# Optimization experiments

Measured on AMD Instinct MI355X. Metric: run time of the kernel, lower is better.

## Reference

```python
import jax, jax.numpy as jnp
import numpy as np

NS = 150            # number of MC weight samples
D_IN, D_H, D_OUT = 1024, 512, 256


def setup_inputs() -> dict:
    key = jax.random.key(0)
    ks = jax.random.split(key, 9)
    x = jax.random.normal(ks[0], (32, D_IN), dtype=jnp.float32)
    # variational means (mu network params)
    mu_W1 = jax.random.normal(ks[1], (D_H, D_IN), dtype=jnp.float32) * 0.02
    mu_b1 = jnp.zeros((D_H,), dtype=jnp.float32)
    mu_W2 = jax.random.normal(ks[2], (D_OUT, D_H), dtype=jnp.float32) * 0.02
    mu_b2 = jnp.zeros((D_OUT,), dtype=jnp.float32)
    # variational log-stds (std network params v); std = exp(v)
    v_W1 = -3.0 + 0.1 * jax.random.normal(ks[3], (D_H, D_IN), dtype=jnp.float32)
    v_b1 = -3.0 + 0.1 * jax.random.normal(ks[4], (D_H,), dtype=jnp.float32)
    v_W2 = -3.0 + 0.1 * jax.random.normal(ks[5], (D_OUT, D_H), dtype=jnp.float32)
    v_b2 = -3.0 + 0.1 * jax.random.normal(ks[6], (D_OUT,), dtype=jnp.float32)
    return {
        "x": x,
        "mu_W1": mu_W1, "mu_b1": mu_b1, "mu_W2": mu_W2, "mu_b2": mu_b2,
        "v_W1": v_W1, "v_b1": v_b1, "v_W2": v_W2, "v_b2": v_b2,
    }


def reference(x, mu_W1, mu_b1, mu_W2, mu_b2, v_W1, v_b1, v_W2, v_b2):
    # Reparameterization: w = mu + eps * sqrt(exp(2v)) = mu + eps * exp(v)
    nk = jax.random.split(jax.random.key(42), 4)
    eW1 = jax.random.normal(nk[0], (NS,) + mu_W1.shape, dtype=mu_W1.dtype)
    eb1 = jax.random.normal(nk[1], (NS,) + mu_b1.shape, dtype=mu_b1.dtype)
    eW2 = jax.random.normal(nk[2], (NS,) + mu_W2.shape, dtype=mu_W2.dtype)
    eb2 = jax.random.normal(nk[3], (NS,) + mu_b2.shape, dtype=mu_b2.dtype)

    W1 = mu_W1 + eW1 * jnp.exp(v_W1)          # [ns, H, I]
    b1 = mu_b1 + eb1 * jnp.exp(v_b1)          # [ns, H]
    W2 = mu_W2 + eW2 * jnp.exp(v_W2)          # [ns, O, H]
    b2 = mu_b2 + eb2 * jnp.exp(v_b2)          # [ns, O]

    # MLP forward, batched over the ns sample axis
    h = jax.nn.relu(jnp.einsum('bi,nhi->nbh', x, W1) + b1[:, None, :])  # [ns, B, H]
    y = jnp.einsum('nbh,noh->nbo', h, W2) + b2[:, None, :]              # [ns, B, O]
    return y  # stacked MC outputs, [ns, B, O]
```

## Files before the change

### kernel.cpp

```cpp
#include <hip/hip_runtime.h>
#include <stdint.h>

#define NS 150
#define D_IN 1024
#define D_H 512
#define D_OUT 256

typedef __bf16 bf16x8 __attribute__((ext_vector_type(8)));
typedef float f32x4 __attribute__((ext_vector_type(4)));

#define OFF_XF    0u
#define OFF_MS1T  16384u
#define OFF_MS2T  1064960u
#define OFF_B1S   1327104u
#define OFF_B2S   1403904u
#define OFF_HB    1442304u

#define SQ2 1.41421354f

#define DSQ2 1.4142135623730951
#define DA  (-0.6931471805599453)
#define ZC3 ((float)(DSQ2 * -4.39150654e-06 * DA*DA*DA*DA*DA))
#define ZC4 ((float)(DSQ2 * 0.00021858087   * DA*DA*DA*DA))
#define ZC5 ((float)(DSQ2 * -0.00125372503  * DA*DA*DA))
#define ZC6 ((float)(DSQ2 * -0.00417768164  * DA*DA))
#define ZC7 ((float)(DSQ2 * 0.246640727     * DA))
#define ZC8 ((float)(DSQ2 * 1.50140941))
#define ZSHIFT 3.6067376022224085f
#define ZCUT  -7.213475204444817f

#define TT0 (SQ2 * -0.000200214257f)
#define TT1 (SQ2 * 0.000100950558f)
#define TT2 (SQ2 * 0.00134934322f)
#define TT3 (SQ2 * -0.00367342844f)
#define TT4 (SQ2 * 0.00573950773f)
#define TT5 (SQ2 * -0.0076224613f)
#define TT6 (SQ2 * 0.00943887047f)
#define TT7 (SQ2 * 1.00167406f)
#define TT8 (SQ2 * 2.83297682f)

#define ROTL32(x, r) __builtin_rotateleft32((x), (r))

__host__ __device__ __forceinline__ void threefry2x32(uint32_t k0, uint32_t k1,
                                                      uint32_t x0, uint32_t x1,
                                                      uint32_t& o0, uint32_t& o1) {
  uint32_t k2 = k0 ^ k1 ^ 0x1BD11BDAu;
  x0 += k0; x1 += k1;
#define TFR(r) { x0 += x1; x1 = ROTL32(x1, r); x1 ^= x0; }
  TFR(13) TFR(15) TFR(26) TFR(6)
  x0 += k1; x1 += k2 + 1u;
  TFR(17) TFR(29) TFR(16) TFR(24)
  x0 += k2; x1 += k0 + 2u;
  TFR(13) TFR(15) TFR(26) TFR(6)
  x0 += k0; x1 += k1 + 3u;
  TFR(17) TFR(29) TFR(16) TFR(24)
  x0 += k1; x1 += k2 + 4u;
  TFR(13) TFR(15) TFR(26) TFR(6)
  x0 += k2; x1 += k0 + 5u;
#undef TFR
  o0 = x0; o1 = x1;
}

__device__ __forceinline__ float tf_normal(uint32_t k0, uint32_t k1, uint32_t idx) {
  uint32_t o0, o1;
  threefry2x32(k0, k1, 0u, idx, o0, o1);
  uint32_t bits = o0 ^ o1;
  uint32_t fb = (bits >> 9) | 0x3F800000u;
  float m = __uint_as_float(fb);
  const float lo = -0.99999994f;
  float u = fmaxf(fmaf(m, 2.0f, -3.0f), lo);
  float t = fmaf(u, -u, 1.0f);
  float w = -0.69314718056f * __builtin_amdgcn_logf(t);
  float p;
  if (w < 5.0f) {
    float ww = w - 2.5f;
    p = SQ2 * 2.81022636e-08f;
    p = fmaf(p, ww, SQ2 * 3.43273939e-07f);
    p = fmaf(p, ww, SQ2 * -3.5233877e-06f);
    p = fmaf(p, ww, SQ2 * -4.39150654e-06f);
    p = fmaf(p, ww, SQ2 * 0.00021858087f);
    p = fmaf(p, ww, SQ2 * -0.00125372503f);
    p = fmaf(p, ww, SQ2 * -0.00417768164f);
    p = fmaf(p, ww, SQ2 * 0.246640727f);
    p = fmaf(p, ww, SQ2 * 1.50140941f);
  } else {
    float ww = __builtin_amdgcn_sqrtf(w) - 3.0f;
    p = TT0;
    p = fmaf(p, ww, TT1); p = fmaf(p, ww, TT2); p = fmaf(p, ww, TT3);
    p = fmaf(p, ww, TT4); p = fmaf(p, ww, TT5); p = fmaf(p, ww, TT6);
    p = fmaf(p, ww, TT7); p = fmaf(p, ww, TT8);
  }
  return p * u;
}

#define TF_ADD8 \
  "v_add_u32 %[a0], %[a0], %[b0]\n\t" "v_add_u32 %[a1], %[a1], %[b1]\n\t" \
  "v_add_u32 %[a2], %[a2], %[b2]\n\t" "v_add_u32 %[a3], %[a3], %[b3]\n\t" \
  "v_add_u32 %[a4], %[a4], %[b4]\n\t" "v_add_u32 %[a5], %[a5], %[b5]\n\t" \
  "v_add_u32 %[a6], %[a6], %[b6]\n\t" "v_add_u32 %[a7], %[a7], %[b7]\n\t"
#define TF_ROT8(sh) \
  "v_alignbit_b32 %[b0], %[b0], %[b0], " sh "\n\t" \
  "v_alignbit_b32 %[b1], %[b1], %[b1], " sh "\n\t" \
  "v_alignbit_b32 %[b2], %[b2], %[b2], " sh "\n\t" \
  "v_alignbit_b32 %[b3], %[b3], %[b3], " sh "\n\t" \
  "v_alignbit_b32 %[b4], %[b4], %[b4], " sh "\n\t" \
  "v_alignbit_b32 %[b5], %[b5], %[b5], " sh "\n\t" \
  "v_alignbit_b32 %[b6], %[b6], %[b6], " sh "\n\t" \
  "v_alignbit_b32 %[b7], %[b7], %[b7], " sh "\n\t"
#define TF_XOR8 \
  "v_xor_b32 %[b0], %[b0], %[a0]\n\t" "v_xor_b32 %[b1], %[b1], %[a1]\n\t" \
  "v_xor_b32 %[b2], %[b2], %[a2]\n\t" "v_xor_b32 %[b3], %[b3], %[a3]\n\t" \
  "v_xor_b32 %[b4], %[b4], %[a4]\n\t" "v_xor_b32 %[b5], %[b5], %[a5]\n\t" \
  "v_xor_b32 %[b6], %[b6], %[a6]\n\t" "v_xor_b32 %[b7], %[b7], %[a7]\n\t"
#define TF_ROUND(sh) TF_ADD8 TF_ROT8(sh) TF_XOR8
#define TF_R1(sh) \
  "v_add_u32 %[a0], %[k0], %[b0]\n\t" "v_add_u32 %[a1], %[k0], %[b1]\n\t" \
  "v_add_u32 %[a2], %[k0], %[b2]\n\t" "v_add_u32 %[a3], %[k0], %[b3]\n\t" \
  "v_add_u32 %[a4], %[k0], %[b4]\n\t" "v_add_u32 %[a5], %[k0], %[b5]\n\t" \
  "v_add_u32 %[a6], %[k0], %[b6]\n\t" "v_add_u32 %[a7], %[k0], %[b7]\n\t" \
  TF_ROT8(sh) TF_XOR8
#define TF_BADD8(KB) \
  "v_add_u32 %[b0], " KB ", %[b0]\n\t" "v_add_u32 %[b1], " KB ", %[b1]\n\t" \
  "v_add_u32 %[b2], " KB ", %[b2]\n\t" "v_add_u32 %[b3], " KB ", %[b3]\n\t" \
  "v_add_u32 %[b4], " KB ", %[b4]\n\t" "v_add_u32 %[b5], " KB ", %[b5]\n\t" \
  "v_add_u32 %[b6], " KB ", %[b6]\n\t" "v_add_u32 %[b7], " KB ", %[b7]\n\t"
#define TF_AADD8(KA) \
  "v_add_u32 %[a0], " KA ", %[a0]\n\t" "v_add_u32 %[a1], " KA ", %[a1]\n\t" \
  "v_add_u32 %[a2], " KA ", %[a2]\n\t" "v_add_u32 %[a3], " KA ", %[a3]\n\t" \
  "v_add_u32 %[a4], " KA ", %[a4]\n\t" "v_add_u32 %[a5], " KA ", %[a5]\n\t" \
  "v_add_u32 %[a6], " KA ", %[a6]\n\t" "v_add_u32 %[a7], " KA ", %[a7]\n\t"
#define TF_A3F(KA) \
  "v_add3_u32 %[a0], %[a0], %[b0], " KA "\n\t" \
  "v_add3_u32 %[a1], %[a1], %[b1], " KA "\n\t" \
  "v_add3_u32 %[a2], %[a2], %[b2], " KA "\n\t" \
  "v_add3_u32 %[a3], %[a3], %[b3], " KA "\n\t" \
  "v_add3_u32 %[a4], %[a4], %[b4], " KA "\n\t" \
  "v_add3_u32 %[a5], %[a5], %[b5], " KA "\n\t" \
  "v_add3_u32 %[a6], %[a6], %[b6], " KA "\n\t" \
  "v_add3_u32 %[a7], %[a7], %[b7], " KA "\n\t"
#define TF_RFOLD(KB, KA, sh) TF_BADD8(KB) TF_A3F(KA) TF_ROT8(sh) TF_XOR8

__device__ __forceinline__ void tf8_bits(uint32_t k0, uint32_t k1, uint32_t k2,
                                         uint32_t idx0, uint32_t* bits) {
  uint32_t k2p1 = k2 + 1u, k0p2 = k0 + 2u, k1p3 = k1 + 3u;
  uint32_t k2p4 = k2 + 4u, k0p5 = k0 + 5u;
  uint32_t t0 = idx0 + k1;
  uint32_t a0, a1, a2, a3, a4, a5, a6, a7;
  uint32_t b0 = t0, b1 = t0 + 1u, b2 = t0 + 2u, b3 = t0 + 3u;
  uint32_t b4 = t0 + 4u, b5 = t0 + 5u, b6 = t0 + 6u, b7 = t0 + 7u;
  asm(TF_R1("19") TF_ROUND("17") TF_ROUND("6") TF_ROUND("26")
      TF_RFOLD("%[k2p1]", "%[k1]", "15")
      TF_ROUND("3") TF_ROUND("16") TF_ROUND("8")
      TF_RFOLD("%[k0p2]", "%[k2]", "19")
      TF_ROUND("17") TF_ROUND("6") TF_ROUND("26")
      TF_RFOLD("%[k1p3]", "%[k0]", "15")
      TF_ROUND("3") TF_ROUND("16") TF_ROUND("8")
      TF_RFOLD("%[k2p4]", "%[k1]", "19")
      TF_ROUND("17") TF_ROUND("6") TF_ROUND("26")
      TF_AADD8("%[k2]") TF_BADD8("%[k0p5]")
      : [a0]"=&v"(a0), [a1]"=&v"(a1), [a2]"=&v"(a2), [a3]"=&v"(a3),
        [a4]"=&v"(a4), [a5]"=&v"(a5), [a6]"=&v"(a6), [a7]"=&v"(a7),
        [b0]"+v"(b0), [b1]"+v"(b1), [b2]"+v"(b2), [b3]"+v"(b3),
        [b4]"+v"(b4), [b5]"+v"(b5), [b6]"+v"(b6), [b7]"+v"(b7)
      : [k0]"s"(k0), [k1]"s"(k1), [k2]"s"(k2), [k2p1]"s"(k2p1),
        [k0p2]"s"(k0p2), [k1p3]"s"(k1p3), [k2p4]"s"(k2p4), [k0p5]"s"(k0p5));
  bits[0] = a0 ^ b0; bits[1] = a1 ^ b1; bits[2] = a2 ^ b2; bits[3] = a3 ^ b3;
  bits[4] = a4 ^ b4; bits[5] = a5 ^ b5; bits[6] = a6 ^ b6; bits[7] = a7 ^ b7;
}

__device__ __forceinline__ float bits_normal(uint32_t bits) {
  uint32_t fb = (bits >> 9) | 0x3F800000u;
  float m = __uint_as_float(fb);
  const float lo = -0.99999994f;
  float u = fmaxf(fmaf(m, 2.0f, -3.0f), lo);
  float t = fmaf(u, -u, 1.0f);
  float z = __builtin_amdgcn_logf(t);
  float p;
  if (z > ZCUT) {
    float zz = z + ZSHIFT;
    p = ZC3;
    p = fmaf(p, zz, ZC4); p = fmaf(p, zz, ZC5); p = fmaf(p, zz, ZC6);
    p = fmaf(p, zz, ZC7); p = fmaf(p, zz, ZC8);
  } else {
    float w = -0.69314718056f * z;
    float ww = __builtin_amdgcn_sqrtf(w) - 3.0f;
    p = TT0;
    p = fmaf(p, ww, TT1); p = fmaf(p, ww, TT2); p = fmaf(p, ww, TT3);
    p = fmaf(p, ww, TT4); p = fmaf(p, ww, TT5); p = fmaf(p, ww, TT6);
    p = fmaf(p, ww, TT7); p = fmaf(p, ww, TT8);
  }
  return p * u;
}

__global__ __launch_bounds__(256) void prep_kernel(
    const float* __restrict__ x,
    const float* __restrict__ muW1, const float* __restrict__ vW1,
    const float* __restrict__ muW2, const float* __restrict__ vW2,
    const float* __restrict__ mub1, const float* __restrict__ vb1,
    const float* __restrict__ mub2, const float* __restrict__ vb2,
    float* __restrict__ ws,
    uint32_t kb1_0, uint32_t kb1_1, uint32_t kb2_0, uint32_t kb2_1) {
  int bb = blockIdx.x;
  int tid = threadIdx.x;
  if (bb < 2048) {
    int t = bb * 256 + tid;
    ((float2*)(ws + OFF_MS1T))[t] = make_float2(muW1[t], expf(vW1[t]));
  } else if (bb < 2560) {
    int t = (bb - 2048) * 256 + tid;
    ((float2*)(ws + OFF_MS2T))[t] = make_float2(muW2[t], expf(vW2[t]));
  } else if (bb < 2688) {
    int t = (bb - 2560) * 256 + tid;
    int j = t & 7, lane = (t >> 3) & 63, fidx = t >> 9;
    int s = fidx >> 1, f = fidx & 1;
    int b = f * 16 + (lane & 15);
    int k = s * 32 + ((lane >> 4) << 3) + j;
    ((__bf16*)(ws + OFF_XF))[t] = (__bf16)x[b * D_IN + k];
  } else if (bb < 2988) {
    int t = (bb - 2688) * 256 + tid;
    int h = t & 511;
    float eps = tf_normal(kb1_0, kb1_1, (uint32_t)t);
    ws[OFF_B1S + t] = fmaf(eps, expf(vb1[h]), mub1[h]);
  } else {
    int t = (bb - 2988) * 256 + tid;
    int o = t & 255;
    float eps = tf_normal(kb2_0, kb2_1, (uint32_t)t);
    ws[OFF_B2S + t] = fmaf(eps, expf(vb2[o]), mub2[o]);
  }
}

__global__ __launch_bounds__(128) void l1_kernel(
    const float* __restrict__ ws, uint32_t k0, uint32_t k1) {
  const float2* __restrict__ ms1 = (const float2*)(ws + OFF_MS1T);
  const bf16x8* __restrict__ xf = (const bf16x8*)(ws + OFF_XF);
  const float* __restrict__ b1s = ws + OFF_B1S;
  __bf16* __restrict__ hB = (__bf16*)(ws + OFF_HB);
  uint32_t k2 = k0 ^ k1 ^ 0x1BD11BDAu;

  __shared__ f32x4 lred[2][64];

  int lane = threadIdx.x & 63;
  int khalf = threadIdx.x >> 6;
  int tile = blockIdx.x;
  int n = tile >> 5;
  int ht = tile & 31;
  int mrow = lane & 15, quad = lane >> 4;
  int h = ht * 16 + mrow;
  uint32_t base = ((uint32_t)(n * 512 + h)) << 10;
  const float2* __restrict__ msrow = ms1 + (size_t)h * D_IN;

  f32x4 acc0 = {0.f, 0.f, 0.f, 0.f}, acc1 = {0.f, 0.f, 0.f, 0.f};

  int send = khalf * 16 + 16;
  for (int s = khalf * 16; s < send; ++s) {
    int kq = s * 32 + quad * 8;
    const f32x4* msq = (const f32x4*)(msrow + kq);
    f32x4 q0 = msq[0], q1 = msq[1], q2 = msq[2], q3 = msq[3];
    bf16x8 b0 = xf[(s * 2 + 0) * 64 + lane];
    bf16x8 b1 = xf[(s * 2 + 1) * 64 + lane];
    uint32_t bits[8];
    tf8_bits(k0, k1, k2, base + (uint32_t)kq, bits);
    float mu[8], sd[8];
    mu[0]=q0[0]; sd[0]=q0[1]; mu[1]=q0[2]; sd[1]=q0[3];
    mu[2]=q1[0]; sd[2]=q1[1]; mu[3]=q1[2]; sd[3]=q1[3];
    mu[4]=q2[0]; sd[4]=q2[1]; mu[5]=q2[2]; sd[5]=q2[3];
    mu[6]=q3[0]; sd[6]=q3[1]; mu[7]=q3[2]; sd[7]=q3[3];
    bf16x8 a;
#pragma unroll
    for (int j = 0; j < 8; ++j) {
      float eps = bits_normal(bits[j]);
      a[j] = (__bf16)fmaf(eps, sd[j], mu[j]);
    }
    acc0 = __builtin_amdgcn_mfma_f32_16x16x32_bf16(a, b0, acc0, 0, 0, 0);
    acc1 = __builtin_amdgcn_mfma_f32_16x16x32_bf16(a, b1, acc1, 0, 0, 0);
  }

  if (khalf) {
    lred[0][lane] = acc0;
    lred[1][lane] = acc1;
  }
  __syncthreads();
  if (!khalf) {
    f32x4 r0 = lred[0][lane], r1 = lred[1][lane];
    acc0 += r0; acc1 += r1;
    int hq = ht * 16 + quad * 4;
    float4 bias = *(const float4*)(b1s + n * 512 + hq);
    float bv[4] = {bias.x, bias.y, bias.z, bias.w};
    union { __bf16 v[4]; uint2 u; } p0, p1;
#pragma unroll
    for (int r = 0; r < 4; ++r) {
      p0.v[r] = (__bf16)fmaxf(acc0[r] + bv[r], 0.0f);
      p1.v[r] = (__bf16)fmaxf(acc1[r] + bv[r], 0.0f);
    }
    size_t o0 = ((((size_t)(n * 16 + (ht >> 1)) * 2 + 0) * 4 +
                  ((ht & 1) * 2 + (quad >> 1))) * 16 + mrow) * 8 + (quad & 1) * 4;
    *(uint2*)(hB + o0) = p0.u;
    *(uint2*)(hB + o0 + 512) = p1.u;
  }
}

__global__ __launch_bounds__(128) void l2_kernel(
    const float* __restrict__ ws, float* __restrict__ y,
    uint32_t k0, uint32_t k1) {
  const float2* __restrict__ ms2 = (const float2*)(ws + OFF_MS2T);
  const bf16x8* __restrict__ hB8 = (const bf16x8*)(ws + OFF_HB);
  const float* __restrict__ b2s = ws + OFF_B2S;
  uint32_t k2 = k0 ^ k1 ^ 0x1BD11BDAu;

  __shared__ f32x4 lred[2][64];

  int lane = threadIdx.x & 63;
  int khalf = threadIdx.x >> 6;
  int tile = blockIdx.x;
  int n = tile >> 4;
  int ot = tile & 15;
  int mrow = lane & 15, quad = lane >> 4;
  int o = ot * 16 + mrow;
  uint32_t base = (uint32_t)(n * 256 + o) << 9;
  const float2* __restrict__ msrow = ms2 + (size_t)o * D_H;

  f32x4 acc0 = {0.f, 0.f, 0.f, 0.f}, acc1 = {0.f, 0.f, 0.f, 0.f};

  int send = khalf * 8 + 8;
  for (int s = khalf * 8; s < send; ++s) {
    int kq = s * 32 + quad * 8;
    const f32x4* msq = (const f32x4*)(msrow + kq);
    f32x4 q0 = msq[0], q1 = msq[1], q2 = msq[2], q3 = msq[3];
    const bf16x8* hf = hB8 + (size_t)((n * 16 + s) * 2) * 64;
    bf16x8 b0 = hf[lane];
    bf16x8 b1 = hf[64 + lane];
    uint32_t bits[8];
    tf8_bits(k0, k1, k2, base + (uint32_t)kq, bits);
    float mu[8], sd[8];
    mu[0]=q0[0]; sd[0]=q0[1]; mu[1]=q0[2]; sd[1]=q0[3];
    mu[2]=q1[0]; sd[2]=q1[1]; mu[3]=q1[2]; sd[3]=q1[3];
    mu[4]=q2[0]; sd[4]=q2[1]; mu[5]=q2[2]; sd[5]=q2[3];
    mu[6]=q3[0]; sd[6]=q3[1]; mu[7]=q3[2]; sd[7]=q3[3];
    bf16x8 a;
#pragma unroll
    for (int j = 0; j < 8; ++j) {
      float eps = bits_normal(bits[j]);
      a[j] = (__bf16)fmaf(eps, sd[j], mu[j]);
    }
    acc0 = __builtin_amdgcn_mfma_f32_16x16x32_bf16(a, b0, acc0, 0, 0, 0);
    acc1 = __builtin_amdgcn_mfma_f32_16x16x32_bf16(a, b1, acc1, 0, 0, 0);
  }

  if (khalf) {
    lred[0][lane] = acc0;
    lred[1][lane] = acc1;
  }
  __syncthreads();
  if (!khalf) {
    f32x4 r0 = lred[0][lane], r1 = lred[1][lane];
    acc0 += r0; acc1 += r1;
    int oq = ot * 16 + quad * 4;
    float4 bias = *(const float4*)(b2s + n * 256 + oq);
    float4 o0, o1;
    o0.x = acc0[0] + bias.x; o0.y = acc0[1] + bias.y;
    o0.z = acc0[2] + bias.z; o0.w = acc0[3] + bias.w;
    o1.x = acc1[0] + bias.x; o1.y = acc1[1] + bias.y;
    o1.z = acc1[2] + bias.z; o1.w = acc1[3] + bias.w;
    *(float4*)(y + (size_t)(n * 32 + mrow) * 256 + oq) = o0;
    *(float4*)(y + (size_t)(n * 32 + 16 + mrow) * 256 + oq) = o1;
  }
}

extern "C" void kernel_launch(void* const* d_in, const int* in_sizes, int n_in,
                              void* d_out, int out_size, void* d_ws, size_t ws_size,
                              hipStream_t stream) {
  const float* x = (const float*)d_in[0];
  const float* muW1 = (const float*)d_in[1];
  const float* mub1 = (const float*)d_in[2];
  const float* muW2 = (const float*)d_in[3];
  const float* mub2 = (const float*)d_in[4];
  const float* vW1 = (const float*)d_in[5];
  const float* vb1 = (const float*)d_in[6];
  const float* vW2 = (const float*)d_in[7];
  const float* vb2 = (const float*)d_in[8];
  float* y = (float*)d_out;
  float* ws = (float*)d_ws;

  uint32_t nk[4][2];
  for (uint32_t j = 0; j < 4; ++j) {
    threefry2x32(0u, 42u, 0u, j, nk[j][0], nk[j][1]);
  }

  prep_kernel<<<3138, 256, 0, stream>>>(
      x, muW1, vW1, muW2, vW2, mub1, vb1, mub2, vb2, ws,
      nk[1][0], nk[1][1], nk[3][0], nk[3][1]);

  l1_kernel<<<4800, 128, 0, stream>>>(ws, nk[0][0], nk[0][1]);

  l2_kernel<<<2400, 128, 0, stream>>>(ws, y, nk[2][0], nk[2][1]);
}
```

Measured before the change: 301.0 us.

## Compute exp(v) inline in GEMM kernels instead of precomputing interleaved mu/std arrays

Removes the prep pass that wrote interleaved (mu, exp(v)) float2 arrays for W1 and W2. The layer kernels now read mu and v directly from the inputs and compute the std with a hardware exp2 per element. The b2 sampling work moves into extra blocks of the l1 kernel, so prep shrinks to the x conversion and b1. This drops roughly 10MB of workspace write and read traffic and shortens a kernel, at the cost of an exp2 per weight element in each of the 150 samples.

After: 314.0 us. 1.04x slower.

```diff
diff --git a/kernel.cpp b/kernel.cpp
--- a/kernel.cpp
+++ b/kernel.cpp
@@ -10,11 +10,11 @@
 typedef float f32x4 __attribute__((ext_vector_type(4)));
 
 #define OFF_XF    0u
-#define OFF_MS1T  16384u
-#define OFF_MS2T  1064960u
-#define OFF_B1S   1327104u
-#define OFF_B2S   1403904u
-#define OFF_HB    1442304u
+#define OFF_B1S   16384u
+#define OFF_B2S   93184u
+#define OFF_HB    131584u
+
+#define LOG2E 1.44269504f
 
 #define SQ2 1.41421354f
 
@@ -194,46 +194,42 @@
 
 __global__ __launch_bounds__(256) void prep_kernel(
     const float* __restrict__ x,
-    const float* __restrict__ muW1, const float* __restrict__ vW1,
-    const float* __restrict__ muW2, const float* __restrict__ vW2,
     const float* __restrict__ mub1, const float* __restrict__ vb1,
-    const float* __restrict__ mub2, const float* __restrict__ vb2,
     float* __restrict__ ws,
-    uint32_t kb1_0, uint32_t kb1_1, uint32_t kb2_0, uint32_t kb2_1) {
+    uint32_t kb1_0, uint32_t kb1_1) {
   int bb = blockIdx.x;
   int tid = threadIdx.x;
-  if (bb < 2048) {
+  if (bb < 128) {
     int t = bb * 256 + tid;
-    ((float2*)(ws + OFF_MS1T))[t] = make_float2(muW1[t], expf(vW1[t]));
-  } else if (bb < 2560) {
-    int t = (bb - 2048) * 256 + tid;
-    ((float2*)(ws + OFF_MS2T))[t] = make_float2(muW2[t], expf(vW2[t]));
-  } else if (bb < 2688) {
-    int t = (bb - 2560) * 256 + tid;
     int j = t & 7, lane = (t >> 3) & 63, fidx = t >> 9;
     int s = fidx >> 1, f = fidx & 1;
     int b = f * 16 + (lane & 15);
     int k = s * 32 + ((lane >> 4) << 3) + j;
     ((__bf16*)(ws + OFF_XF))[t] = (__bf16)x[b * D_IN + k];
-  } else if (bb < 2988) {
-    int t = (bb - 2688) * 256 + tid;
+  } else {
+    int t = (bb - 128) * 256 + tid;
     int h = t & 511;
     float eps = tf_normal(kb1_0, kb1_1, (uint32_t)t);
     ws[OFF_B1S + t] = fmaf(eps, expf(vb1[h]), mub1[h]);
-  } else {
-    int t = (bb - 2988) * 256 + tid;
+  }
+}
+
+__global__ __launch_bounds__(128) void l1_kernel(
+    const float* __restrict__ ws,
+    const float* __restrict__ muW1, const float* __restrict__ vW1,
+    const float* __restrict__ mub2, const float* __restrict__ vb2,
+    float* __restrict__ wsout,
+    uint32_t k0, uint32_t k1, uint32_t kb2_0, uint32_t kb2_1) {
+  if (blockIdx.x >= 4800) {
+    int t = (blockIdx.x - 4800) * 128 + threadIdx.x;
     int o = t & 255;
     float eps = tf_normal(kb2_0, kb2_1, (uint32_t)t);
-    ws[OFF_B2S + t] = fmaf(eps, expf(vb2[o]), mub2[o]);
-  }
-}
-
-__global__ __launch_bounds__(128) void l1_kernel(
-    const float* __restrict__ ws, uint32_t k0, uint32_t k1) {
-  const float2* __restrict__ ms1 = (const float2*)(ws + OFF_MS1T);
+    wsout[OFF_B2S + t] = fmaf(eps, expf(vb2[o]), mub2[o]);
+    return;
+  }
   const bf16x8* __restrict__ xf = (const bf16x8*)(ws + OFF_XF);
   const float* __restrict__ b1s = ws + OFF_B1S;
-  __bf16* __restrict__ hB = (__bf16*)(ws + OFF_HB);
+  __bf16* __restrict__ hB = (__bf16*)(wsout + OFF_HB);
   uint32_t k2 = k0 ^ k1 ^ 0x1BD11BDAu;
 
   __shared__ f32x4 lred[2][64];
@@ -246,29 +242,33 @@
   int mrow = lane & 15, quad = lane >> 4;
   int h = ht * 16 + mrow;
   uint32_t base = ((uint32_t)(n * 512 + h)) << 10;
-  const float2* __restrict__ msrow = ms1 + (size_t)h * D_IN;
+  const float* __restrict__ mu1row = muW1 + (size_t)h * D_IN;
+  const float* __restrict__ v1row  = vW1  + (size_t)h * D_IN;
 
   f32x4 acc0 = {0.f, 0.f, 0.f, 0.f}, acc1 = {0.f, 0.f, 0.f, 0.f};
 
   int send = khalf * 16 + 16;
   for (int s = khalf * 16; s < send; ++s) {
     int kq = s * 32 + quad * 8;
-    const f32x4* msq = (const f32x4*)(msrow + kq);
-    f32x4 q0 = msq[0], q1 = msq[1], q2 = msq[2], q3 = msq[3];
+    const f32x4* muq = (const f32x4*)(mu1row + kq);
+    const f32x4* vq  = (const f32x4*)(v1row + kq);
+    f32x4 m0 = muq[0], m1 = muq[1];
+    f32x4 w0 = vq[0],  w1 = vq[1];
     bf16x8 b0 = xf[(s * 2 + 0) * 64 + lane];
     bf16x8 b1 = xf[(s * 2 + 1) * 64 + lane];
     uint32_t bits[8];
     tf8_bits(k0, k1, k2, base + (uint32_t)kq, bits);
     float mu[8], sd[8];
-    mu[0]=q0[0]; sd[0]=q0[1]; mu[1]=q0[2]; sd[1]=q0[3];
-    mu[2]=q1[0]; sd[2]=q1[1]; mu[3]=q1[2]; sd[3]=q1[3];
-    mu[4]=q2[0]; sd[4]=q2[1]; mu[5]=q2[2]; sd[5]=q2[3];
-    mu[6]=q3[0]; sd[6]=q3[1]; mu[7]=q3[2]; sd[7]=q3[3];
+    mu[0]=m0[0]; mu[1]=m0[1]; mu[2]=m0[2]; mu[3]=m0[3];
+    mu[4]=m1[0]; mu[5]=m1[1]; mu[6]=m1[2]; mu[7]=m1[3];
+    sd[0]=w0[0]; sd[1]=w0[1]; sd[2]=w0[2]; sd[3]=w0[3];
+    sd[4]=w1[0]; sd[5]=w1[1]; sd[6]=w1[2]; sd[7]=w1[3];
     bf16x8 a;
 #pragma unroll
     for (int j = 0; j < 8; ++j) {
       float eps = bits_normal(bits[j]);
-      a[j] = (__bf16)fmaf(eps, sd[j], mu[j]);
+      float st = __builtin_amdgcn_exp2f(sd[j] * LOG2E);
+      a[j] = (__bf16)fmaf(eps, st, mu[j]);
     }
     acc0 = __builtin_amdgcn_mfma_f32_16x16x32_bf16(a, b0, acc0, 0, 0, 0);
     acc1 = __builtin_amdgcn_mfma_f32_16x16x32_bf16(a, b1, acc1, 0, 0, 0);
@@ -299,9 +299,10 @@
 }
 
 __global__ __launch_bounds__(128) void l2_kernel(
-    const float* __restrict__ ws, float* __restrict__ y,
+    const float* __restrict__ ws,
+    const float* __restrict__ muW2, const float* __restrict__ vW2,
+    float* __restrict__ y,
     uint32_t k0, uint32_t k1) {
-  const float2* __restrict__ ms2 = (const float2*)(ws + OFF_MS2T);
   const bf16x8* __restrict__ hB8 = (const bf16x8*)(ws + OFF_HB);
   const float* __restrict__ b2s = ws + OFF_B2S;
   uint32_t k2 = k0 ^ k1 ^ 0x1BD11BDAu;
@@ -316,30 +317,34 @@
   int mrow = lane & 15, quad = lane >> 4;
   int o = ot * 16 + mrow;
   uint32_t base = (uint32_t)(n * 256 + o) << 9;
-  const float2* __restrict__ msrow = ms2 + (size_t)o * D_H;
+  const float* __restrict__ mu2row = muW2 + (size_t)o * D_H;
+  const float* __restrict__ v2row  = vW2  + (size_t)o * D_H;
 
   f32x4 acc0 = {0.f, 0.f, 0.f, 0.f}, acc1 = {0.f, 0.f, 0.f, 0.f};
 
   int send = khalf * 8 + 8;
   for (int s = khalf * 8; s < send; ++s) {
     int kq = s * 32 + quad * 8;
-    const f32x4* msq = (const f32x4*)(msrow + kq);
-    f32x4 q0 = msq[0], q1 = msq[1], q2 = msq[2], q3 = msq[3];
+    const f32x4* muq = (const f32x4*)(mu2row + kq);
+    const f32x4* vq  = (const f32x4*)(v2row + kq);
+    f32x4 m0 = muq[0], m1 = muq[1];
+    f32x4 w0 = vq[0],  w1 = vq[1];
     const bf16x8* hf = hB8 + (size_t)((n * 16 + s) * 2) * 64;
     bf16x8 b0 = hf[lane];
     bf16x8 b1 = hf[64 + lane];
     uint32_t bits[8];
     tf8_bits(k0, k1, k2, base + (uint32_t)kq, bits);
     float mu[8], sd[8];
-    mu[0]=q0[0]; sd[0]=q0[1]; mu[1]=q0[2]; sd[1]=q0[3];
-    mu[2]=q1[0]; sd[2]=q1[1]; mu[3]=q1[2]; sd[3]=q1[3];
-    mu[4]=q2[0]; sd[4]=q2[1]; mu[5]=q2[2]; sd[5]=q2[3];
-    mu[6]=q3[0]; sd[6]=q3[1]; mu[7]=q3[2]; sd[7]=q3[3];
+    mu[0]=m0[0]; mu[1]=m0[1]; mu[2]=m0[2]; mu[3]=m0[3];
+    mu[4]=m1[0]; mu[5]=m1[1]; mu[6]=m1[2]; mu[7]=m1[3];
+    sd[0]=w0[0]; sd[1]=w0[1]; sd[2]=w0[2]; sd[3]=w0[3];
+    sd[4]=w1[0]; sd[5]=w1[1]; sd[6]=w1[2]; sd[7]=w1[3];
     bf16x8 a;
 #pragma unroll
     for (int j = 0; j < 8; ++j) {
       float eps = bits_normal(bits[j]);
-      a[j] = (__bf16)fmaf(eps, sd[j], mu[j]);
+      float st = __builtin_amdgcn_exp2f(sd[j] * LOG2E);
+      a[j] = (__bf16)fmaf(eps, st, mu[j]);
     }
     acc0 = __builtin_amdgcn_mfma_f32_16x16x32_bf16(a, b0, acc0, 0, 0, 0);
     acc1 = __builtin_amdgcn_mfma_f32_16x16x32_bf16(a, b1, acc1, 0, 0, 0);
@@ -385,11 +390,13 @@
     threefry2x32(0u, 42u, 0u, j, nk[j][0], nk[j][1]);
   }
 
-  prep_kernel<<<3138, 256, 0, stream>>>(
-      x, muW1, vW1, muW2, vW2, mub1, vb1, mub2, vb2, ws,
-      nk[1][0], nk[1][1], nk[3][0], nk[3][1]);
-
-  l1_kernel<<<4800, 128, 0, stream>>>(ws, nk[0][0], nk[0][1]);
-
-  l2_kernel<<<2400, 128, 0, stream>>>(ws, y, nk[2][0], nk[2][1]);
-}
+  prep_kernel<<<428, 256, 0, stream>>>(
+      x, mub1, vb1, ws, nk[1][0], nk[1][1]);
+
+  l1_kernel<<<5100, 128, 0, stream>>>(
+      ws, muW1, vW1, mub2, vb2, ws,
+      nk[0][0], nk[0][1], nk[3][0], nk[3][1]);
+
+  l2_kernel<<<2400, 128, 0, stream>>>(
+      ws, muW2, vW2, y, nk[2][0], nk[2][1]);
+}
```

## Move layer-2 weight and bias prep into l1 launch; pack two tiles per l2 block

Applied to the files above, without the earlier changes.

The layer-2 mean/std packing and the b2 sampling move out of the prep kernel and into extra trailing blocks of the layer-1 kernel, so that work runs alongside layer-1 tiles instead of before them. This shortens the serial prep stage. The layer-2 kernel now runs 256-thread blocks that each handle two output tiles, halving its block count and sharing one sync. The l1 kernel takes separate input and output workspace pointers that alias the same buffer, so correctness relies on the regions not overlapping.

Result: no change. 297.5 us (-1.2%).

```diff
diff --git a/kernel.cpp b/kernel.cpp
--- a/kernel.cpp
+++ b/kernel.cpp
@@ -195,45 +195,55 @@
 __global__ __launch_bounds__(256) void prep_kernel(
     const float* __restrict__ x,
     const float* __restrict__ muW1, const float* __restrict__ vW1,
-    const float* __restrict__ muW2, const float* __restrict__ vW2,
     const float* __restrict__ mub1, const float* __restrict__ vb1,
-    const float* __restrict__ mub2, const float* __restrict__ vb2,
     float* __restrict__ ws,
-    uint32_t kb1_0, uint32_t kb1_1, uint32_t kb2_0, uint32_t kb2_1) {
+    uint32_t kb1_0, uint32_t kb1_1) {
   int bb = blockIdx.x;
   int tid = threadIdx.x;
   if (bb < 2048) {
     int t = bb * 256 + tid;
     ((float2*)(ws + OFF_MS1T))[t] = make_float2(muW1[t], expf(vW1[t]));
-  } else if (bb < 2560) {
+  } else if (bb < 2176) {
     int t = (bb - 2048) * 256 + tid;
-    ((float2*)(ws + OFF_MS2T))[t] = make_float2(muW2[t], expf(vW2[t]));
-  } else if (bb < 2688) {
-    int t = (bb - 2560) * 256 + tid;
     int j = t & 7, lane = (t >> 3) & 63, fidx = t >> 9;
     int s = fidx >> 1, f = fidx & 1;
     int b = f * 16 + (lane & 15);
     int k = s * 32 + ((lane >> 4) << 3) + j;
     ((__bf16*)(ws + OFF_XF))[t] = (__bf16)x[b * D_IN + k];
-  } else if (bb < 2988) {
-    int t = (bb - 2688) * 256 + tid;
+  } else {
+    int t = (bb - 2176) * 256 + tid;
     int h = t & 511;
     float eps = tf_normal(kb1_0, kb1_1, (uint32_t)t);
     ws[OFF_B1S + t] = fmaf(eps, expf(vb1[h]), mub1[h]);
-  } else {
-    int t = (bb - 2988) * 256 + tid;
+  }
+}
+
+__global__ __launch_bounds__(128) void l1_kernel(
+    const float* __restrict__ ws,
+    const float* __restrict__ muW2, const float* __restrict__ vW2,
+    const float* __restrict__ mub2, const float* __restrict__ vb2,
+    float* __restrict__ wsout,
+    uint32_t k0, uint32_t k1, uint32_t kb2_0, uint32_t kb2_1) {
+  if (blockIdx.x >= 5312) {
+    int t = (blockIdx.x - 5312) * 128 + threadIdx.x;
     int o = t & 255;
     float eps = tf_normal(kb2_0, kb2_1, (uint32_t)t);
-    ws[OFF_B2S + t] = fmaf(eps, expf(vb2[o]), mub2[o]);
-  }
-}
-
-__global__ __launch_bounds__(128) void l1_kernel(
-    const float* __restrict__ ws, uint32_t k0, uint32_t k1) {
+    wsout[OFF_B2S + t] = fmaf(eps, expf(vb2[o]), mub2[o]);
+    return;
+  }
+  if (blockIdx.x >= 4800) {
+    int t = ((blockIdx.x - 4800) * 128 + threadIdx.x) * 2;
+    float2 mu2 = *(const float2*)(muW2 + t);
+    float2 v2  = *(const float2*)(vW2 + t);
+    float2* ms2 = (float2*)(wsout + OFF_MS2T);
+    ms2[t]     = make_float2(mu2.x, expf(v2.x));
+    ms2[t + 1] = make_float2(mu2.y, expf(v2.y));
+    return;
+  }
   const float2* __restrict__ ms1 = (const float2*)(ws + OFF_MS1T);
   const bf16x8* __restrict__ xf = (const bf16x8*)(ws + OFF_XF);
   const float* __restrict__ b1s = ws + OFF_B1S;
-  __bf16* __restrict__ hB = (__bf16*)(ws + OFF_HB);
+  __bf16* __restrict__ hB = (__bf16*)(wsout + OFF_HB);
   uint32_t k2 = k0 ^ k1 ^ 0x1BD11BDAu;
 
   __shared__ f32x4 lred[2][64];
@@ -298,7 +308,7 @@
   }
 }
 
-__global__ __launch_bounds__(128) void l2_kernel(
+__global__ __launch_bounds__(256) void l2_kernel(
     const float* __restrict__ ws, float* __restrict__ y,
     uint32_t k0, uint32_t k1) {
   const float2* __restrict__ ms2 = (const float2*)(ws + OFF_MS2T);
@@ -306,11 +316,12 @@
   const float* __restrict__ b2s = ws + OFF_B2S;
   uint32_t k2 = k0 ^ k1 ^ 0x1BD11BDAu;
 
-  __shared__ f32x4 lred[2][64];
+  __shared__ f32x4 lred[2][2][64];
 
   int lane = threadIdx.x & 63;
-  int khalf = threadIdx.x >> 6;
-  int tile = blockIdx.x;
+  int wib = threadIdx.x >> 6;
+  int pairIdx = wib >> 1, khalf = wib & 1;
+  int tile = blockIdx.x * 2 + pairIdx;
   int n = tile >> 4;
   int ot = tile & 15;
   int mrow = lane & 15, quad = lane >> 4;
@@ -346,12 +357,12 @@
   }
 
   if (khalf) {
-    lred[0][lane] = acc0;
-    lred[1][lane] = acc1;
+    lred[pairIdx][0][lane] = acc0;
+    lred[pairIdx][1][lane] = acc1;
   }
   __syncthreads();
   if (!khalf) {
-    f32x4 r0 = lred[0][lane], r1 = lred[1][lane];
+    f32x4 r0 = lred[pairIdx][0][lane], r1 = lred[pairIdx][1][lane];
     acc0 += r0; acc1 += r1;
     int oq = ot * 16 + quad * 4;
     float4 bias = *(const float4*)(b2s + n * 256 + oq);
@@ -385,11 +396,12 @@
     threefry2x32(0u, 42u, 0u, j, nk[j][0], nk[j][1]);
   }
 
-  prep_kernel<<<3138, 256, 0, stream>>>(
-      x, muW1, vW1, muW2, vW2, mub1, vb1, mub2, vb2, ws,
-      nk[1][0], nk[1][1], nk[3][0], nk[3][1]);
-
-  l1_kernel<<<4800, 128, 0, stream>>>(ws, nk[0][0], nk[0][1]);
-
-  l2_kernel<<<2400, 128, 0, stream>>>(ws, y, nk[2][0], nk[2][1]);
-}
+  prep_kernel<<<2476, 256, 0, stream>>>(
+      x, muW1, vW1, mub1, vb1, ws, nk[1][0], nk[1][1]);
+
+  l1_kernel<<<5612, 128, 0, stream>>>(
+      ws, muW2, vW2, mub2, vb2, ws,
+      nk[0][0], nk[0][1], nk[3][0], nk[3][1]);
+
+  l2_kernel<<<1200, 256, 0, stream>>>(ws, y, nk[2][0], nk[2][1]);
+}
```
